# Performance work log

Hardware: AMD Instinct MI355X
Metric: run time of the kernel (lower is better)

Reference implementation:

```python
import jax, jax.numpy as jnp
import numpy as np

DIM = 1024


def setup_inputs() -> dict:
    key = jax.random.key(0)
    ks = jax.random.split(key, 10)
    B, S, D = 4, 2048, DIM
    std = 1.0 / np.sqrt(D)  # torch Linear default uniform bound
    return {
        "query": jax.random.normal(ks[0], (B, S, D), jnp.float32),
        "key": jax.random.normal(ks[1], (B, S, D), jnp.float32),
        "value": jax.random.normal(ks[2], (B, S, D), jnp.float32),
        "context": jnp.zeros((D,), jnp.float32),
        "Wq": jax.random.uniform(ks[3], (D, D), jnp.float32, -std, std),
        "bq": jax.random.uniform(ks[4], (D,), jnp.float32, -std, std),
        "Wk": jax.random.uniform(ks[5], (D, D), jnp.float32, -std, std),
        "bk": jax.random.uniform(ks[6], (D,), jnp.float32, -std, std),
        "Wv": jax.random.uniform(ks[7], (D, D), jnp.float32, -std, std),
        "bv": jax.random.uniform(ks[8], (D,), jnp.float32, -std, std),
    }


def reference(query, key, value, context, Wq, bq, Wk, bk, Wv, bv):
    scale = query.shape[-1] ** -0.5
    # torch Linear: x @ W.T + b
    q = (query + context) @ Wq.T + bq          # [B,S,D]
    k = (key + context) @ Wk.T + bk            # [B,S,D]
    v = value @ Wv.T + bv                      # [B,S,D]
    scores = jnp.einsum("bqd,bkd->bqk", q, k) * scale  # [B,S,S]
    weights = jax.nn.softmax(scores, axis=-1)
    return jnp.einsum("bqk,bkd->bqd", weights, v)
```

## Files before the change

### kernel.cpp

```cpp
#include <hip/hip_runtime.h>

typedef __attribute__((ext_vector_type(8))) short bf16x8;
typedef __attribute__((ext_vector_type(4))) float floatx4;

constexpr int BATCH = 4;
constexpr int SEQ   = 2048;
constexpr int DIMN  = 1024;
constexpr int M1    = BATCH * SEQ;

constexpr int BM = 128, BK = 32;

__device__ __forceinline__ short f2bf(float f) {
    union { float f; unsigned u; } x; x.f = f;
    unsigned r = x.u + 0x7fffu + ((x.u >> 16) & 1u);
    return (short)(r >> 16);
}
__device__ __forceinline__ float bf2f(short s) {
    union { unsigned u; float f; } x; x.u = ((unsigned)(unsigned short)s) << 16;
    return x.f;
}

__device__ __forceinline__ void async16(const void* g, void* l) {
    __builtin_amdgcn_global_load_lds(
        (const __attribute__((address_space(1))) unsigned int*)g,
        (__attribute__((address_space(3))) unsigned int*)l, 16, 0, 0);
}

template<bool OUT_BF16, int WJ>
__device__ __forceinline__ void gemm_core(
    const short* __restrict__ Ab, int lda,
    const short* __restrict__ Bb, int ldb,
    void* __restrict__ Cb, int ldc,
    const float* __restrict__ bias, int K, float scale,
    int m0, int n0)
{
    constexpr int BN_ = WJ * 32;
    __shared__ short As[2][BM][BK];
    __shared__ short Bs[2][BN_][BK];

    const int tid  = threadIdx.x;
    const int lane = tid & 63;
    const int wave = tid >> 6;
    const int wr = wave >> 1, wc = wave & 1;
    const int lr = lane & 15;
    const int lq = lane >> 4;

    const int row = tid >> 2;
    const int kc  = (tid & 3) * 8;
    const short* pA = Ab + (size_t)(m0 + row) * lda + kc;
    const short* pB = Bb + (size_t)(n0 + row) * ldb + kc;
    const size_t stA = (size_t)64 * lda;
    const size_t stB = (size_t)64 * ldb;

    floatx4 acc[4][WJ];
    #pragma unroll
    for (int i = 0; i < 4; ++i)
        #pragma unroll
        for (int j = 0; j < WJ; ++j) acc[i][j] = (floatx4)(0.f);

    auto stage = [&](int bi) {
        async16(pA,       &As[bi][row][kc]);
        async16(pA + stA, &As[bi][row + 64][kc]);
        async16(pB,       &Bs[bi][row][kc]);
        if (WJ == 4) async16(pB + stB, &Bs[bi][row + 64][kc]);
        pA += BK; pB += BK;
    };

    const int NK = K / BK;
    stage(0);
    __syncthreads();

    for (int it = 0; it < NK; ++it) {
        const int bi = it & 1;
        if (it + 1 < NK) stage(bi ^ 1);

        bf16x8 af[4], bfr[WJ];
        #pragma unroll
        for (int i = 0; i < 4; ++i)
            af[i] = *(const bf16x8*)&As[bi][wr * 64 + i * 16 + lr][lq * 8];
        #pragma unroll
        for (int j = 0; j < WJ; ++j)
            bfr[j] = *(const bf16x8*)&Bs[bi][wc * (16 * WJ) + j * 16 + lr][lq * 8];
        #pragma unroll
        for (int i = 0; i < 4; ++i)
            #pragma unroll
            for (int j = 0; j < WJ; ++j)
                acc[i][j] = __builtin_amdgcn_mfma_f32_16x16x32_bf16(
                    af[i], bfr[j], acc[i][j], 0, 0, 0);

        if (it + 1 < NK) __syncthreads();
    }

    #pragma unroll
    for (int j = 0; j < WJ; ++j) {
        const int gn = n0 + wc * (16 * WJ) + j * 16 + lr;
        const float bv = bias ? bias[gn] : 0.f;
        #pragma unroll
        for (int i = 0; i < 4; ++i) {
            #pragma unroll
            for (int r = 0; r < 4; ++r) {
                const int gm = m0 + wr * 64 + i * 16 + lq * 4 + r;
                const float v = acc[i][j][r] * scale + bv;
                if (OUT_BF16) {
                    ((short*)Cb)[(size_t)gm * ldc + gn] = f2bf(v);
                } else {
                    ((float*)Cb)[(size_t)gm * ldc + gn] = v;
                }
            }
        }
    }
}

__global__ __launch_bounds__(256)
void proj_qkv(const short* __restrict__ xq, const short* __restrict__ xk,
              const short* __restrict__ xv,
              const short* __restrict__ Wq_, const short* __restrict__ Wk_,
              const short* __restrict__ Wv_,
              const float* __restrict__ bq_, const float* __restrict__ bk_,
              const float* __restrict__ bv_,
              short* __restrict__ q, short* __restrict__ k, short* __restrict__ vp)
{
    const int b   = blockIdx.x;
    const int xcd = b & 7;
    const int i   = b >> 3;
    const int z   = i >> 6;
    const int mm  = (i >> 3) & 7;
    const int nn  = i & 7;
    const short* X = (z == 0) ? xq : (z == 1) ? xk : xv;
    const short* W = (z == 0) ? Wq_ : (z == 1) ? Wk_ : Wv_;
    const float* bb = (z == 0) ? bq_ : (z == 1) ? bk_ : bv_;
    short* O = (z == 0) ? q : (z == 1) ? k : vp;
    gemm_core<true, 4>(X, DIMN, W, DIMN, (void*)O, DIMN, bb, DIMN, 1.f,
                       (xcd * 8 + mm) * BM, nn * 128);
}

__global__ __launch_bounds__(256)
void gemm_scores(const short* __restrict__ q, const short* __restrict__ k,
                 short* __restrict__ S, float scale)
{
    const int b   = blockIdx.x;
    const int xcd = b & 7;
    const int i   = b >> 3;
    const int bz  = xcd >> 1;
    const int mh  = xcd & 1;
    const int mm  = i >> 4;
    const int nn  = i & 15;
    gemm_core<true, 4>(q + (size_t)bz * SEQ * DIMN, DIMN,
                       k + (size_t)bz * SEQ * DIMN, DIMN,
                       (void*)(S + (size_t)bz * SEQ * SEQ), SEQ,
                       nullptr, DIMN, scale,
                       (mh * 8 + mm) * BM, nn * 128);
}

__global__ __launch_bounds__(256)
void gemm_pv(const short* __restrict__ P, const short* __restrict__ vt,
             float* __restrict__ O)
{
    const int b   = blockIdx.x;
    const int xcd = b & 7;
    const int i   = b >> 3;
    const int bz  = xcd >> 1;
    const int mh  = xcd & 1;
    const int mm  = i >> 4;
    const int nn  = i & 15;
    gemm_core<false, 2>(P  + (size_t)bz * SEQ * SEQ,  SEQ,
                        vt + (size_t)bz * DIMN * SEQ, SEQ,
                        (void*)(O + (size_t)bz * SEQ * DIMN), DIMN,
                        nullptr, SEQ, 1.f,
                        (mh * 8 + mm) * BM, nn * 64);
}

__global__ __launch_bounds__(256)
void cvt_tri(const float* __restrict__ in0, short* __restrict__ out0,
             const float* __restrict__ in1, short* __restrict__ out1,
             const float* __restrict__ in2, short* __restrict__ out2, int n8)
{
    const int z = blockIdx.z;
    const float* in = (z == 0) ? in0 : (z == 1) ? in1 : in2;
    short* out      = (z == 0) ? out0 : (z == 1) ? out1 : out2;
    const int i = blockIdx.x * 256 + threadIdx.x;
    if (i >= n8) return;
    const float4 a0 = ((const float4*)in)[(size_t)i * 2];
    const float4 a1 = ((const float4*)in)[(size_t)i * 2 + 1];
    const float v[8] = {a0.x, a0.y, a0.z, a0.w, a1.x, a1.y, a1.z, a1.w};
    bf16x8 o;
    #pragma unroll
    for (int j = 0; j < 8; ++j) o[j] = f2bf(v[j]);
    *(bf16x8*)(out + (size_t)i * 8) = o;
}

__global__ __launch_bounds__(256)
void bias3(const float* __restrict__ Wq, const float* __restrict__ Wk,
           const float* __restrict__ Wv,
           const float* __restrict__ bq, const float* __restrict__ bk,
           const float* __restrict__ bv,
           const float* __restrict__ ctx,
           float* __restrict__ oq, float* __restrict__ ok, float* __restrict__ ov)
{
    const int z = blockIdx.y;
    const float* W = (z == 0) ? Wq : (z == 1) ? Wk : Wv;
    const float* b = (z == 0) ? bq : (z == 1) ? bk : bv;
    float*       o = (z == 0) ? oq : (z == 1) ? ok : ov;
    const int n    = blockIdx.x * 4 + (threadIdx.x >> 6);
    const int lane = threadIdx.x & 63;
    float s = 0.f;
    if (z < 2) {
        const float* row = W + (size_t)n * DIMN;
        for (int k = lane * 4; k < DIMN; k += 256) {
            const float4 x = *(const float4*)(row + k);
            const float4 c = *(const float4*)(ctx + k);
            s += x.x * c.x + x.y * c.y + x.z * c.z + x.w * c.w;
        }
        #pragma unroll
        for (int off = 32; off > 0; off >>= 1) s += __shfl_xor(s, off);
    }
    if (lane == 0) o[n] = b[n] + s;
}

__global__ __launch_bounds__(256)
void transpose_v(const short* __restrict__ in, short* __restrict__ out)
{
    __shared__ short t[64][68];
    const int b  = blockIdx.z;
    const int d0 = blockIdx.x * 64;
    const int s0 = blockIdx.y * 64;
    const int r  = threadIdx.x >> 3;
    const int c  = (threadIdx.x & 7) * 8;
    #pragma unroll
    for (int h = 0; h < 2; ++h) {
        const int s = r + h * 32;
        bf16x8 v = *(const bf16x8*)(in + ((size_t)b * SEQ + s0 + s) * DIMN + d0 + c);
        #pragma unroll
        for (int j = 0; j < 8; ++j) t[c + j][s] = v[j];
    }
    __syncthreads();
    #pragma unroll
    for (int h = 0; h < 2; ++h) {
        const int d = r + h * 32;
        bf16x8 v;
        #pragma unroll
        for (int j = 0; j < 8; ++j) v[j] = t[d][c + j];
        *(bf16x8*)(out + ((size_t)b * DIMN + d0 + d) * SEQ + s0 + c) = v;
    }
}

__global__ __launch_bounds__(256)
void softmax_kernel(short* __restrict__ P)
{
    const int bid = blockIdx.x;
    const int xcd = bid & 7;
    const int i   = bid >> 3;
    const int row = (xcd >> 1) * SEQ + (xcd & 1) * 1024 + i;
    short* p = P + (size_t)row * SEQ;
    const int t    = threadIdx.x;
    const int lane = t & 63;
    const int wave = t >> 6;
    __shared__ float red[8];

    bf16x8 raw = *(const bf16x8*)(p + t * 8);
    float v[8];
    float mx = -1e30f;
    #pragma unroll
    for (int j = 0; j < 8; ++j) { v[j] = bf2f(raw[j]); mx = fmaxf(mx, v[j]); }
    #pragma unroll
    for (int off = 32; off > 0; off >>= 1) mx = fmaxf(mx, __shfl_xor(mx, off));
    if (lane == 0) red[wave] = mx;
    __syncthreads();
    mx = fmaxf(fmaxf(red[0], red[1]), fmaxf(red[2], red[3]));

    float e[8], s = 0.f;
    #pragma unroll
    for (int j = 0; j < 8; ++j) { e[j] = __expf(v[j] - mx); s += e[j]; }
    #pragma unroll
    for (int off = 32; off > 0; off >>= 1) s += __shfl_xor(s, off);
    if (lane == 0) red[4 + wave] = s;
    __syncthreads();
    s = red[4] + red[5] + red[6] + red[7];
    const float inv = 1.f / s;

    bf16x8 o;
    #pragma unroll
    for (int j = 0; j < 8; ++j) o[j] = f2bf(e[j] * inv);
    *(bf16x8*)(p + t * 8) = o;
}

extern "C" void kernel_launch(void* const* d_in, const int* in_sizes, int n_in,
                              void* d_out, int out_size, void* d_ws, size_t ws_size,
                              hipStream_t stream)
{
    const float* query = (const float*)d_in[0];
    const float* key_  = (const float*)d_in[1];
    const float* value = (const float*)d_in[2];
    const float* ctx   = (const float*)d_in[3];
    const float* Wq    = (const float*)d_in[4];
    const float* bq    = (const float*)d_in[5];
    const float* Wk    = (const float*)d_in[6];
    const float* bk    = (const float*)d_in[7];
    const float* Wv    = (const float*)d_in[8];
    const float* bv    = (const float*)d_in[9];

    char* ws = (char*)d_ws;
    char* od = (char*)d_out;
    const size_t MB = 1ull << 20;
    short* xq   = (short*)(ws);
    short* xk   = (short*)(ws + 16 * MB);
    short* q_b  = (short*)(ws + 32 * MB);
    short* k_b  = (short*)(ws + 48 * MB);
    short* Wq_b = (short*)(ws + 64 * MB);
    short* Wk_b = (short*)(ws + 66 * MB);
    short* Wv_b = (short*)(ws + 68 * MB);
    float* bq_e = (float*)(ws + 70 * MB);
    float* bk_e = (float*)(ws + 70 * MB + 4096);
    float* bv_e = (float*)(ws + 70 * MB + 8192);
    short* S_b  = (short*)(ws);
    short* v_t  = (short*)(ws + 64 * MB);
    short* xv   = (short*)(od);
    short* vp   = (short*)(od + 16 * MB);

    dim3 blk(256);
    const int W8 = DIMN * DIMN / 8;
    const int X8 = M1 * DIMN / 8;

    cvt_tri<<<dim3(W8 / 256, 1, 3), blk, 0, stream>>>(Wq, Wq_b, Wk, Wk_b, Wv, Wv_b, W8);
    bias3<<<dim3(DIMN / 4, 3), blk, 0, stream>>>(Wq, Wk, Wv, bq, bk, bv, ctx,
                                                 bq_e, bk_e, bv_e);
    cvt_tri<<<dim3(X8 / 256, 1, 3), blk, 0, stream>>>(query, xq, key_, xk, value, xv, X8);

    proj_qkv<<<dim3(1536), blk, 0, stream>>>(xq, xk, xv, Wq_b, Wk_b, Wv_b,
                                             bq_e, bk_e, bv_e, q_b, k_b, vp);
    transpose_v<<<dim3(DIMN / 64, SEQ / 64, BATCH), blk, 0, stream>>>(vp, v_t);

    const float scale = 1.0f / 32.0f;
    gemm_scores<<<dim3(1024), blk, 0, stream>>>(q_b, k_b, S_b, scale);

    softmax_kernel<<<dim3(M1), blk, 0, stream>>>(S_b);

    gemm_pv<<<dim3(1024), blk, 0, stream>>>(S_b, v_t, (float*)d_out);
}
```

Baseline: 345.2 us.

## Replace GEMM core with 256x128 tile, 8-wave, triple-buffered swizzled pipeline

```diff
diff --git a/kernel.cpp b/kernel.cpp
--- a/kernel.cpp
+++ b/kernel.cpp
@@ -8,8 +8,6 @@
 constexpr int DIMN  = 1024;
 constexpr int M1    = BATCH * SEQ;
 
-constexpr int BM = 128, BK = 32;
-
 __device__ __forceinline__ short f2bf(float f) {
     union { float f; unsigned u; } x; x.f = f;
     unsigned r = x.u + 0x7fffu + ((x.u >> 16) & 1u);
@@ -26,92 +24,135 @@
         (__attribute__((address_space(3))) unsigned int*)l, 16, 0, 0);
 }
 
-template<bool OUT_BF16, int WJ>
-__device__ __forceinline__ void gemm_core(
+#define WAITVM(N) asm volatile("s_waitcnt vmcnt(" #N ")" ::: "memory")
+#define MEMFENCE  asm volatile("" ::: "memory")
+
+template<bool OUT_BF16>
+__device__ __forceinline__ void gemm256(
     const short* __restrict__ Ab, int lda,
     const short* __restrict__ Bb, int ldb,
     void* __restrict__ Cb, int ldc,
     const float* __restrict__ bias, int K, float scale,
     int m0, int n0)
 {
-    constexpr int BN_ = WJ * 32;
-    __shared__ short As[2][BM][BK];
-    __shared__ short Bs[2][BN_][BK];
-
-    const int tid  = threadIdx.x;
-    const int lane = tid & 63;
-    const int wave = tid >> 6;
-    const int wr = wave >> 1, wc = wave & 1;
-    const int lr = lane & 15;
-    const int lq = lane >> 4;
-
-    const int row = tid >> 2;
-    const int kc  = (tid & 3) * 8;
-    const short* pA = Ab + (size_t)(m0 + row) * lda + kc;
-    const short* pB = Bb + (size_t)(n0 + row) * ldb + kc;
-    const size_t stA = (size_t)64 * lda;
-    const size_t stB = (size_t)64 * ldb;
-
-    floatx4 acc[4][WJ];
-    #pragma unroll
-    for (int i = 0; i < 4; ++i)
-        #pragma unroll
-        for (int j = 0; j < WJ; ++j) acc[i][j] = (floatx4)(0.f);
-
-    auto stage = [&](int bi) {
-        async16(pA,       &As[bi][row][kc]);
-        async16(pA + stA, &As[bi][row + 64][kc]);
-        async16(pB,       &Bs[bi][row][kc]);
-        if (WJ == 4) async16(pB + stB, &Bs[bi][row + 64][kc]);
-        pA += BK; pB += BK;
+    __shared__ alignas(16) char smem[3][49152];
+
+    const int t    = threadIdx.x;
+    const int lane = t & 63;
+    const int wave = t >> 6;
+    const int wr   = wave >> 2;
+    const int wc   = wave & 3;
+    const int lr   = lane & 15;
+    const int lq   = lane >> 4;
+
+    const short* pA[4];
+    const short* pB[2];
+    #pragma unroll
+    for (int s = 0; s < 4; ++s) {
+        const int P = s * 8192 + t * 16;
+        const int L = P ^ (((P >> 7) & 7) << 4);
+        pA[s] = Ab + (size_t)(m0 + (L >> 7)) * lda + ((L & 127) >> 1);
+    }
+    #pragma unroll
+    for (int s = 0; s < 2; ++s) {
+        const int P = s * 8192 + t * 16;
+        const int L = P ^ (((P >> 7) & 7) << 4);
+        pB[s] = Bb + (size_t)(n0 + (L >> 7)) * ldb + ((L & 127) >> 1);
+    }
+
+    int roA[8], roB[2], colp[2];
+    #pragma unroll
+    for (int m = 0; m < 8; ++m) roA[m] = (wr * 128 + m * 16 + lr) * 128;
+    #pragma unroll
+    for (int n = 0; n < 2; ++n) roB[n] = 32768 + (wc * 32 + n * 16 + lr) * 128;
+    #pragma unroll
+    for (int kk = 0; kk < 2; ++kk)
+        colp[kk] = ((kk << 6) | (lq << 4)) ^ ((lane & 7) << 4);
+
+    floatx4 acc[8][2];
+    #pragma unroll
+    for (int m = 0; m < 8; ++m)
+        #pragma unroll
+        for (int n = 0; n < 2; ++n) acc[m][n] = (floatx4)(0.f);
+
+    const int ldst = t * 16;
+    auto stage_a = [&](int sb) {
+        char* base = smem[sb];
+        async16(pA[0], base +          ldst);
+        async16(pA[1], base +  8192 + ldst);
+        async16(pA[2], base + 16384 + ldst);
+        pA[0] += 64; pA[1] += 64; pA[2] += 64;
     };
-
-    const int NK = K / BK;
-    stage(0);
-    __syncthreads();
-
-    for (int it = 0; it < NK; ++it) {
-        const int bi = it & 1;
-        if (it + 1 < NK) stage(bi ^ 1);
-
-        bf16x8 af[4], bfr[WJ];
-        #pragma unroll
-        for (int i = 0; i < 4; ++i)
-            af[i] = *(const bf16x8*)&As[bi][wr * 64 + i * 16 + lr][lq * 8];
-        #pragma unroll
-        for (int j = 0; j < WJ; ++j)
-            bfr[j] = *(const bf16x8*)&Bs[bi][wc * (16 * WJ) + j * 16 + lr][lq * 8];
-        #pragma unroll
-        for (int i = 0; i < 4; ++i)
+    auto stage_b = [&](int sb) {
+        char* base = smem[sb];
+        async16(pA[3], base + 24576 + ldst);
+        async16(pB[0], base + 32768 + ldst);
+        async16(pB[1], base + 40960 + ldst);
+        pA[3] += 64; pB[0] += 64; pB[1] += 64;
+    };
+    auto compute = [&](int buf, int kk) {
+        const char* base = smem[buf];
+        bf16x8 a[8], bfr[2];
+        #pragma unroll
+        for (int m = 0; m < 8; ++m)
+            a[m] = *(const bf16x8*)(base + roA[m] + colp[kk]);
+        #pragma unroll
+        for (int n = 0; n < 2; ++n)
+            bfr[n] = *(const bf16x8*)(base + roB[n] + colp[kk]);
+        __builtin_amdgcn_s_setprio(1);
+        #pragma unroll
+        for (int m = 0; m < 8; ++m)
             #pragma unroll
-            for (int j = 0; j < WJ; ++j)
-                acc[i][j] = __builtin_amdgcn_mfma_f32_16x16x32_bf16(
-                    af[i], bfr[j], acc[i][j], 0, 0, 0);
-
-        if (it + 1 < NK) __syncthreads();
-    }
-
-    #pragma unroll
-    for (int j = 0; j < WJ; ++j) {
-        const int gn = n0 + wc * (16 * WJ) + j * 16 + lr;
+            for (int n = 0; n < 2; ++n)
+                acc[m][n] = __builtin_amdgcn_mfma_f32_16x16x32_bf16(
+                    a[m], bfr[n], acc[m][n], 0, 0, 0);
+        __builtin_amdgcn_s_setprio(0);
+    };
+
+    const int NT = K >> 6;
+    stage_a(0); stage_b(0);
+    stage_a(1); stage_b(1);
+
+    int buf = 0;
+    for (int tt = 0; tt < NT; ++tt) {
+        const int  sb  = (buf == 0) ? 2 : buf - 1;
+        const bool stg = (tt + 2) < NT;
+        if (stg) stage_a(sb);
+        if (tt + 2 < NT)      { WAITVM(9); }
+        else if (tt + 1 < NT) { WAITVM(6); }
+        else                  { WAITVM(0); }
+        __builtin_amdgcn_s_barrier();
+        MEMFENCE;
+        compute(buf, 0);
+        MEMFENCE;
+        __builtin_amdgcn_s_barrier();
+        if (stg) stage_b(sb);
+        __builtin_amdgcn_s_barrier();
+        MEMFENCE;
+        compute(buf, 1);
+        MEMFENCE;
+        __builtin_amdgcn_s_barrier();
+        buf = (buf == 2) ? 0 : buf + 1;
+    }
+
+    #pragma unroll
+    for (int n = 0; n < 2; ++n) {
+        const int gn = n0 + wc * 32 + n * 16 + lr;
         const float bv = bias ? bias[gn] : 0.f;
         #pragma unroll
-        for (int i = 0; i < 4; ++i) {
+        for (int m = 0; m < 8; ++m) {
             #pragma unroll
             for (int r = 0; r < 4; ++r) {
-                const int gm = m0 + wr * 64 + i * 16 + lq * 4 + r;
-                const float v = acc[i][j][r] * scale + bv;
-                if (OUT_BF16) {
-                    ((short*)Cb)[(size_t)gm * ldc + gn] = f2bf(v);
-                } else {
-                    ((float*)Cb)[(size_t)gm * ldc + gn] = v;
-                }
+                const int gm = m0 + wr * 128 + m * 16 + lq * 4 + r;
+                const float v = acc[m][n][r] * scale + bv;
+                if (OUT_BF16) ((short*)Cb)[(size_t)gm * ldc + gn] = f2bf(v);
+                else          ((float*)Cb)[(size_t)gm * ldc + gn] = v;
             }
         }
     }
 }
 
-__global__ __launch_bounds__(256)
+__global__ __launch_bounds__(512)
 void proj_qkv(const short* __restrict__ xq, const short* __restrict__ xk,
               const short* __restrict__ xv,
               const short* __restrict__ Wq_, const short* __restrict__ Wk_,
@@ -123,18 +164,19 @@
     const int b   = blockIdx.x;
     const int xcd = b & 7;
     const int i   = b >> 3;
-    const int z   = i >> 6;
-    const int mm  = (i >> 3) & 7;
-    const int nn  = i & 7;
+    const int z   = i >> 5;
+    const int r   = i & 31;
+    const int mm  = r >> 3;
+    const int nn  = r & 7;
     const short* X = (z == 0) ? xq : (z == 1) ? xk : xv;
     const short* W = (z == 0) ? Wq_ : (z == 1) ? Wk_ : Wv_;
     const float* bb = (z == 0) ? bq_ : (z == 1) ? bk_ : bv_;
     short* O = (z == 0) ? q : (z == 1) ? k : vp;
-    gemm_core<true, 4>(X, DIMN, W, DIMN, (void*)O, DIMN, bb, DIMN, 1.f,
-                       (xcd * 8 + mm) * BM, nn * 128);
-}
-
-__global__ __launch_bounds__(256)
+    gemm256<true>(X, DIMN, W, DIMN, (void*)O, DIMN, bb, DIMN, 1.f,
+                  (xcd * 4 + mm) * 256, nn * 128);
+}
+
+__global__ __launch_bounds__(512)
 void gemm_scores(const short* __restrict__ q, const short* __restrict__ k,
                  short* __restrict__ S, float scale)
 {
@@ -145,14 +187,14 @@
     const int mh  = xcd & 1;
     const int mm  = i >> 4;
     const int nn  = i & 15;
-    gemm_core<true, 4>(q + (size_t)bz * SEQ * DIMN, DIMN,
-                       k + (size_t)bz * SEQ * DIMN, DIMN,
-                       (void*)(S + (size_t)bz * SEQ * SEQ), SEQ,
-                       nullptr, DIMN, scale,
-                       (mh * 8 + mm) * BM, nn * 128);
-}
-
-__global__ __launch_bounds__(256)
+    gemm256<true>(q + (size_t)bz * SEQ * DIMN, DIMN,
+                  k + (size_t)bz * SEQ * DIMN, DIMN,
+                  (void*)(S + (size_t)bz * SEQ * SEQ), SEQ,
+                  nullptr, DIMN, scale,
+                  (mh * 4 + mm) * 256, nn * 128);
+}
+
+__global__ __launch_bounds__(512)
 void gemm_pv(const short* __restrict__ P, const short* __restrict__ vt,
              float* __restrict__ O)
 {
@@ -161,13 +203,13 @@
     const int i   = b >> 3;
     const int bz  = xcd >> 1;
     const int mh  = xcd & 1;
-    const int mm  = i >> 4;
-    const int nn  = i & 15;
-    gemm_core<false, 2>(P  + (size_t)bz * SEQ * SEQ,  SEQ,
-                        vt + (size_t)bz * DIMN * SEQ, SEQ,
-                        (void*)(O + (size_t)bz * SEQ * DIMN), DIMN,
-                        nullptr, SEQ, 1.f,
-                        (mh * 8 + mm) * BM, nn * 64);
+    const int mm  = i >> 3;
+    const int nn  = i & 7;
+    gemm256<false>(P  + (size_t)bz * SEQ * SEQ,  SEQ,
+                   vt + (size_t)bz * DIMN * SEQ, SEQ,
+                   (void*)(O + (size_t)bz * SEQ * DIMN), DIMN,
+                   nullptr, SEQ, 1.f,
+                   (mh * 4 + mm) * 256, nn * 128);
 }
 
 __global__ __launch_bounds__(256)
@@ -318,6 +360,7 @@
     short* vp   = (short*)(od + 16 * MB);
 
     dim3 blk(256);
+    dim3 blk512(512);
     const int W8 = DIMN * DIMN / 8;
     const int X8 = M1 * DIMN / 8;
 
@@ -326,14 +369,14 @@
                                                  bq_e, bk_e, bv_e);
     cvt_tri<<<dim3(X8 / 256, 1, 3), blk, 0, stream>>>(query, xq, key_, xk, value, xv, X8);
 
-    proj_qkv<<<dim3(1536), blk, 0, stream>>>(xq, xk, xv, Wq_b, Wk_b, Wv_b,
-                                             bq_e, bk_e, bv_e, q_b, k_b, vp);
+    proj_qkv<<<dim3(768), blk512, 0, stream>>>(xq, xk, xv, Wq_b, Wk_b, Wv_b,
+                                               bq_e, bk_e, bv_e, q_b, k_b, vp);
     transpose_v<<<dim3(DIMN / 64, SEQ / 64, BATCH), blk, 0, stream>>>(vp, v_t);
 
     const float scale = 1.0f / 32.0f;
-    gemm_scores<<<dim3(1024), blk, 0, stream>>>(q_b, k_b, S_b, scale);
+    gemm_scores<<<dim3(512), blk512, 0, stream>>>(q_b, k_b, S_b, scale);
 
     softmax_kernel<<<dim3(M1), blk, 0, stream>>>(S_b);
 
-    gemm_pv<<<dim3(1024), blk, 0, stream>>>(S_b, v_t, (float*)d_out);
-}
+    gemm_pv<<<dim3(256), blk512, 0, stream>>>(S_b, v_t, (float*)d_out);
+}
```

Result: faster. 320.4 us (-7.2%).
